# Performance work log

Hardware: AMD Instinct MI355X
Metric: run time of the kernel (lower is better)

Reference implementation:

```python
import jax, jax.numpy as jnp
import numpy as np

VOCAB, EMBED, EN_H, DE_H, ATTN, LAYERS = 50000, 256, 512, 512, 256, 2
SEQ, BATCH = 1024, 64

def setup_inputs() -> dict:
    key = jax.random.key(0)
    ks = jax.random.split(key, 20)
    n = lambda k, shp: jax.random.normal(k, shp, dtype=jnp.float32)
    inp = {
        "cur_input": jax.random.randint(ks[0], (BATCH,), 0, VOCAB, dtype=jnp.int64) if jax.config.jax_enable_x64 else jax.random.randint(ks[0], (BATCH,), 0, VOCAB, dtype=jnp.int32),
        "h0": n(ks[1], (LAYERS, BATCH, DE_H)),
        "c0": n(ks[2], (LAYERS, BATCH, DE_H)),
        "enc_states": n(ks[3], (SEQ, BATCH, EN_H)),
        "attention_mask": jnp.ones((BATCH, SEQ), dtype=jnp.float32),
        # parameters
        "emb_table": n(ks[4], (VOCAB, EMBED)) * 0.02,
        "attn_W": n(ks[5], (EN_H + DE_H, ATTN)) * 0.02,   # attention_model: Linear(en+de, attn, bias=False)
        "attn_v": n(ks[6], (ATTN,)) * 0.02,               # Linear(attn, 1, bias=False)
        "cg_W": n(ks[7], (DE_H + EMBED + EN_H, EN_H)) * 0.02,  # context gate
        "cg_b": jnp.zeros((EN_H,), dtype=jnp.float32),
        "Wih0": n(ks[8], (4 * DE_H, EN_H + EMBED)) * 0.02,
        "Whh0": n(ks[9], (4 * DE_H, DE_H)) * 0.02,
        "bih0": jnp.zeros((4 * DE_H,), dtype=jnp.float32),
        "bhh0": jnp.zeros((4 * DE_H,), dtype=jnp.float32),
        "Wih1": n(ks[10], (4 * DE_H, DE_H)) * 0.02,
        "Whh1": n(ks[11], (4 * DE_H, DE_H)) * 0.02,
        "bih1": jnp.zeros((4 * DE_H,), dtype=jnp.float32),
        "bhh1": jnp.zeros((4 * DE_H,), dtype=jnp.float32),
        "out_W": n(ks[12], (DE_H, VOCAB)) * 0.02,
        "out_b": jnp.zeros((VOCAB,), dtype=jnp.float32),
    }
    return inp

def _lstm_cell(x, h, c, Wih, Whh, bih, bhh):
    gates = x @ Wih.T + h @ Whh.T + bih + bhh  # (B, 4H), torch gate order i,f,g,o
    i, f, g, o = jnp.split(gates, 4, axis=-1)
    c_new = jax.nn.sigmoid(f) * c + jax.nn.sigmoid(i) * jnp.tanh(g)
    h_new = jax.nn.sigmoid(o) * jnp.tanh(c_new)
    return h_new, c_new

def reference(cur_input, h0, c0, enc_states, attention_mask,
              emb_table, attn_W, attn_v, cg_W, cg_b,
              Wih0, Whh0, bih0, bhh0, Wih1, Whh1, bih1, bhh1,
              out_W, out_b):
    S, B, _ = enc_states.shape
    dec = h0[-1]  # (B, DE_H)
    # Bahdanau attention: score over seq dim
    dec_b = jnp.broadcast_to(dec[None], (S, B, dec.shape[-1]))
    feat = jnp.tanh(jnp.concatenate([enc_states, dec_b], axis=-1) @ attn_W)  # (S,B,ATTN)
    e = feat @ attn_v  # (S,B)
    e = jnp.where(attention_mask.T > 0, e, jnp.float32(-1e9))
    alpha = jax.nn.softmax(e, axis=0)  # (S,B)
    ctx = jnp.einsum('sb,sbh->bh', alpha, enc_states)  # (B, EN_H)
    # embedding + context gate
    emb = emb_table[cur_input]  # (B, EMBED)
    gate = jax.nn.sigmoid(jnp.concatenate([dec, emb, ctx], axis=-1) @ cg_W + cg_b)
    ctx = gate * ctx
    x = jnp.concatenate([emb, ctx], axis=-1)  # (B, EMBED+EN_H)
    # two-layer single-step LSTM
    h1, c1 = _lstm_cell(x, h0[0], c0[0], Wih0, Whh0, bih0, bhh0)
    h2, c2 = _lstm_cell(h1, h0[1], c0[1], Wih1, Whh1, bih1, bhh1)
    out = h2 @ out_W + out_b  # (B, VOCAB)
    return out, jnp.stack([h1, h2]), jnp.stack([c1, c2])
```

## Files before the change

### kernel.cpp

```cpp
#include <hip/hip_runtime.h>
#include <math.h>


typedef __attribute__((ext_vector_type(8))) short short8;
typedef __attribute__((ext_vector_type(4))) float f32x4;

__device__ __forceinline__ float sigf(float x) { return 1.f / (1.f + expf(-x)); }

__device__ __forceinline__ unsigned short f2bf(float f) {
    unsigned int u = __builtin_bit_cast(unsigned int, f);
    unsigned int r = (u + 0x7fffu + ((u >> 16) & 1u)) >> 16;
    return (unsigned short)r;
}

__device__ __forceinline__ float tanh_fast(float x) {
    float t = __expf(2.f * x);
    return 1.f - 2.f * __builtin_amdgcn_rcpf(1.f + t);
}

__global__ void k_prep_conv(const int* __restrict__ cur, const float* __restrict__ h0,
                            const float* __restrict__ emb_table, const float* __restrict__ attn_W,
                            float* __restrict__ X1, float* __restrict__ X2, float* __restrict__ X3,
                            float* __restrict__ decW, unsigned short* __restrict__ Wt) {
    int t = threadIdx.x;
    if (blockIdx.x >= 64) {
        __shared__ float tile[64][65];
        int bx = blockIdx.x - 64;
        int kb = (bx & 7) * 64, nb = (bx >> 3) * 64;
        int r0 = t >> 6, c = t & 63;
#pragma unroll
        for (int i = 0; i < 16; ++i) {
            int r = i * 4 + r0;
            tile[r][c] = attn_W[(size_t)(kb + r) * 256 + nb + c];
        }
        __syncthreads();
#pragma unroll
        for (int i = 0; i < 16; ++i) {
            int r = i * 4 + r0;
            Wt[(size_t)(nb + r) * 512 + kb + c] = f2bf(tile[c][r]);
        }
        return;
    }
    __shared__ float dec_s[512];
    int b = blockIdx.x;
    const float* dec = h0 + (size_t)(64 + b) * 512;
    for (int i = t; i < 512; i += 256) {
        float v = dec[i];
        dec_s[i] = v;
        X1[b * 1280 + i] = v;
        X2[b * 1280 + 768 + i] = h0[(size_t)b * 512 + i];
        X3[b * 1024 + 512 + i] = v;
    }
    int row = cur[b];
    float ev = emb_table[(size_t)row * 256 + t];
    X1[b * 1280 + 512 + t] = ev;
    X2[b * 1280 + t] = ev;
    __syncthreads();
    float acc = 0.f;
    for (int k = 0; k < 512; ++k)
        acc += dec_s[k] * attn_W[(size_t)(512 + k) * 256 + t];
    decW[b * 256 + t] = acc;
}

__global__ __launch_bounds__(256) void k_scores_mfma(
        const float* __restrict__ enc, const unsigned short* __restrict__ Wt,
        const float* __restrict__ attn_v, const float* __restrict__ decW,
        float* __restrict__ e_out) {
    int s = blockIdx.x, t = threadIdx.x;
    __shared__ __align__(16) unsigned short sA[4096];
    __shared__ __align__(16) unsigned short sB[16384];
    const float* arow = enc + (size_t)s * 64 * 512;
    int w = t >> 6, l = t & 63, li = l & 15, lg = l >> 4;
    int sw = (li & 7) << 4;

    f32x4 acc[4][4];
#pragma unroll
    for (int rt = 0; rt < 4; ++rt)
#pragma unroll
        for (int ct = 0; ct < 4; ++ct) acc[rt][ct] = (f32x4){0.f, 0.f, 0.f, 0.f};

    for (int kk = 0; kk < 512; kk += 64) {
        __syncthreads();
#pragma unroll
        for (int i = 0; i < 2; ++i) {
            int idx = i * 256 + t, row = idx >> 3, kg = idx & 7;
            const float* g = arow + row * 512 + kk + kg * 8;
            float4 p0 = *(const float4*)g;
            float4 p1 = *(const float4*)(g + 4);
            uint4 wv;
            wv.x = f2bf(p0.x) | ((unsigned)f2bf(p0.y) << 16);
            wv.y = f2bf(p0.z) | ((unsigned)f2bf(p0.w) << 16);
            wv.z = f2bf(p1.x) | ((unsigned)f2bf(p1.y) << 16);
            wv.w = f2bf(p1.z) | ((unsigned)f2bf(p1.w) << 16);
            int byte = (row * 128 + kg * 16) ^ ((row & 7) << 4);
            *(uint4*)((char*)sA + byte) = wv;
        }
#pragma unroll
        for (int i = 0; i < 8; ++i) {
            int idx = i * 256 + t, n = idx >> 3, kg = idx & 7;
            uint4 wv = *(const uint4*)(Wt + (size_t)n * 512 + kk + kg * 8);
            int byte = (n * 128 + kg * 16) ^ ((n & 7) << 4);
            *(uint4*)((char*)sB + byte) = wv;
        }
        __syncthreads();
#pragma unroll
        for (int ks = 0; ks < 2; ++ks) {
            short8 af[4], bf[4];
#pragma unroll
            for (int rt = 0; rt < 4; ++rt) {
                int row = rt * 16 + li;
                af[rt] = *(short8*)((char*)sA + ((row * 128 + ks * 64 + lg * 16) ^ sw));
            }
#pragma unroll
            for (int ct = 0; ct < 4; ++ct) {
                int n = w * 64 + ct * 16 + li;
                bf[ct] = *(short8*)((char*)sB + ((n * 128 + ks * 64 + lg * 16) ^ sw));
            }
#pragma unroll
            for (int rt = 0; rt < 4; ++rt)
#pragma unroll
                for (int ct = 0; ct < 4; ++ct)
                    acc[rt][ct] = __builtin_amdgcn_mfma_f32_16x16x32_bf16(
                        af[rt], bf[ct], acc[rt][ct], 0, 0, 0);
        }
    }
    float er[4][4];
#pragma unroll
    for (int rt = 0; rt < 4; ++rt)
#pragma unroll
        for (int r = 0; r < 4; ++r) er[rt][r] = 0.f;
#pragma unroll
    for (int ct = 0; ct < 4; ++ct) {
        int a = w * 64 + ct * 16 + li;
        float v = attn_v[a];
#pragma unroll
        for (int rt = 0; rt < 4; ++rt) {
#pragma unroll
            for (int r = 0; r < 4; ++r) {
                int row = rt * 16 + lg * 4 + r;
                float x = acc[rt][ct][r] + decW[row * 256 + a];
                er[rt][r] += tanh_fast(x) * v;
            }
        }
    }
#pragma unroll
    for (int off = 1; off < 16; off <<= 1)
#pragma unroll
        for (int rt = 0; rt < 4; ++rt)
#pragma unroll
            for (int r = 0; r < 4; ++r)
                er[rt][r] += __shfl_xor(er[rt][r], off, 64);
    __syncthreads();
    float* part = (float*)sA;
    if (li == 0) {
#pragma unroll
        for (int rt = 0; rt < 4; ++rt)
#pragma unroll
            for (int r = 0; r < 4; ++r)
                part[w * 64 + rt * 16 + lg * 4 + r] = er[rt][r];
    }
    __syncthreads();
    if (t < 64)
        e_out[t * 1024 + s] = part[t] + part[64 + t] + part[128 + t] + part[192 + t];
}

__global__ __launch_bounds__(512) void k_ctx_partial(const float* __restrict__ ebuf,
        const float* __restrict__ mask, const float* __restrict__ enc,
        float* __restrict__ ctxP) {
    int b = blockIdx.x & 63, sc = blockIdx.x >> 6;
    int t = threadIdx.x;
    __shared__ float al[128];
    __shared__ float red[16];
    float v0 = ebuf[b * 1024 + t];
    float v1 = ebuf[b * 1024 + 512 + t];
    v0 = (mask[b * 1024 + t] > 0.f) ? v0 : -1e9f;
    v1 = (mask[b * 1024 + 512 + t] > 0.f) ? v1 : -1e9f;
    float lmax = fmaxf(v0, v1);
#pragma unroll
    for (int off = 32; off > 0; off >>= 1) lmax = fmaxf(lmax, __shfl_xor(lmax, off, 64));
    if ((t & 63) == 0) red[t >> 6] = lmax;
    __syncthreads();
    float m = red[0];
#pragma unroll
    for (int i = 1; i < 8; ++i) m = fmaxf(m, red[i]);
    float lsum = __expf(v0 - m) + __expf(v1 - m);
#pragma unroll
    for (int off = 32; off > 0; off >>= 1) lsum += __shfl_xor(lsum, off, 64);
    if ((t & 63) == 0) red[8 + (t >> 6)] = lsum;
    __syncthreads();
    float tot = red[8];
#pragma unroll
    for (int i = 1; i < 8; ++i) tot += red[8 + i];
    float inv = 1.f / tot;
    if (t < 128) {
        int s = sc * 128 + t;
        float x = ebuf[b * 1024 + s];
        x = (mask[b * 1024 + s] > 0.f) ? x : -1e9f;
        al[t] = __expf(x - m) * inv;
    }
    __syncthreads();
    const float* base = enc + (((size_t)sc * 128 * 64) + b) * 512 + t;
    float a0 = 0.f, a1 = 0.f, a2 = 0.f, a3 = 0.f;
    for (int s = 0; s < 128; s += 4) {
        float x0 = base[(size_t)(s + 0) * 32768];
        float x1 = base[(size_t)(s + 1) * 32768];
        float x2 = base[(size_t)(s + 2) * 32768];
        float x3 = base[(size_t)(s + 3) * 32768];
        a0 += al[s] * x0; a1 += al[s + 1] * x1; a2 += al[s + 2] * x2; a3 += al[s + 3] * x3;
    }
    ctxP[((size_t)sc * 64 + b) * 512 + t] = a0 + a1 + a2 + a3;
}

__global__ __launch_bounds__(1024) void k_gemm_cg(const float* __restrict__ X,
        const float* __restrict__ ctxP, const float* __restrict__ Wkn,
        float* __restrict__ P) {
    int n0 = blockIdx.x * 64, sp = blockIdx.y;
    int t = threadIdx.x, tc = t & 63, tr = t >> 6;
    __shared__ __align__(16) float As[64 * 68];
    __shared__ __align__(16) float Wc[64 * 68];
    float acc[4] = {0.f, 0.f, 0.f, 0.f};
    for (int c = 0; c < 5; ++c) {
        int k0 = sp * 320 + c * 64;
        __syncthreads();
#pragma unroll
        for (int i = 0; i < 4; ++i) {
            int idx = i * 1024 + t; int row = idx >> 6; int k = idx & 63;
            int gk = k0 + k;
            float v;
            if (gk < 768) {
                v = X[row * 1280 + gk];
            } else {
                int h = gk - 768;
                v = 0.f;
#pragma unroll
                for (int sc = 0; sc < 8; ++sc)
                    v += ctxP[((size_t)sc * 64 + row) * 512 + h];
            }
            As[k * 68 + row] = v;
        }
#pragma unroll
        for (int i = 0; i < 4; ++i) {
            int idx = i * 1024 + t; int k = idx >> 6; int cc = idx & 63;
            Wc[k * 68 + cc] = Wkn[(size_t)(k0 + k) * 512 + n0 + cc];
        }
        __syncthreads();
#pragma unroll 8
        for (int k = 0; k < 64; ++k) {
            float4 a = *(const float4*)&As[k * 68 + 4 * tr];
            float wv = Wc[k * 68 + tc];
            acc[0] += a.x * wv; acc[1] += a.y * wv; acc[2] += a.z * wv; acc[3] += a.w * wv;
        }
    }
    float* Pp = P + (size_t)sp * 64 * 512;
#pragma unroll
    for (int j = 0; j < 4; ++j) Pp[(4 * tr + j) * 512 + n0 + tc] = acc[j];
}

__global__ __launch_bounds__(1024) void k_gemm_lstm(const float* __restrict__ X, int ldx,
        const float* __restrict__ W1, int K1, const float* __restrict__ W2, int K2,
        int kchunks, float* __restrict__ P) {
    int n0 = blockIdx.x * 64, sp = blockIdx.y;
    int t = threadIdx.x, tc = t & 63, tr = t >> 6;
    __shared__ __align__(16) float As[64 * 68];
    __shared__ __align__(16) float Wc[64 * 68];
    float acc[4] = {0.f, 0.f, 0.f, 0.f};
    for (int c = 0; c < kchunks; ++c) {
        int k0 = (sp * kchunks + c) * 64;
        __syncthreads();
#pragma unroll
        for (int i = 0; i < 4; ++i) {
            int idx = i * 1024 + t; int row = idx >> 6; int k = idx & 63;
            As[k * 68 + row] = X[row * ldx + k0 + k];
        }
#pragma unroll
        for (int i = 0; i < 4; ++i) {
            int idx = i * 1024 + t; int cc = idx >> 6; int k = idx & 63;
            int gk = k0 + k; int j = n0 + cc;
            float wv = (gk < K1) ? W1[(size_t)j * K1 + gk] : W2[(size_t)j * K2 + gk - K1];
            Wc[k * 68 + cc] = wv;
        }
        __syncthreads();
#pragma unroll 8
        for (int k = 0; k < 64; ++k) {
            float4 a = *(const float4*)&As[k * 68 + 4 * tr];
            float wv = Wc[k * 68 + tc];
            acc[0] += a.x * wv; acc[1] += a.y * wv; acc[2] += a.z * wv; acc[3] += a.w * wv;
        }
    }
    float* Pp = P + (size_t)sp * 64 * 2048;
#pragma unroll
    for (int j = 0; j < 4; ++j) Pp[(4 * tr + j) * 2048 + n0 + tc] = acc[j];
}

__global__ void k_cg_fin(const float* __restrict__ P, const float* __restrict__ cg_b,
                         const float* __restrict__ ctxP, float* __restrict__ X2) {
    int idx = blockIdx.x * 256 + threadIdx.x;
    int b = idx >> 9, h = idx & 511;
    float g = cg_b[h];
#pragma unroll
    for (int sp = 0; sp < 4; ++sp) g += P[sp * 32768 + idx];
    float ctx = 0.f;
#pragma unroll
    for (int sc = 0; sc < 8; ++sc) ctx += ctxP[((size_t)sc * 64 + b) * 512 + h];
    X2[b * 1280 + 256 + h] = sigf(g) * ctx;
}

__global__ void k_lstm_fin(const float* __restrict__ P, const float* __restrict__ bih,
                           const float* __restrict__ bhh, const float* __restrict__ c0,
                           int layer, float* __restrict__ oh, float* __restrict__ oc,
                           float* __restrict__ X3out) {
    int idx = blockIdx.x * 256 + threadIdx.x;
    int b = idx >> 9, h = idx & 511;
    float gi = bih[h] + bhh[h];
    float gf = bih[512 + h] + bhh[512 + h];
    float gg = bih[1024 + h] + bhh[1024 + h];
    float go = bih[1536 + h] + bhh[1536 + h];
#pragma unroll
    for (int sp = 0; sp < 4; ++sp) {
        const float* Pp = P + sp * 131072 + b * 2048;
        gi += Pp[h]; gf += Pp[512 + h]; gg += Pp[1024 + h]; go += Pp[1536 + h];
    }
    float cp = c0[layer * 32768 + b * 512 + h];
    float cn = sigf(gf) * cp + sigf(gi) * tanhf(gg);
    float hn = sigf(go) * tanhf(cn);
    oh[b * 512 + h] = hn;
    oc[b * 512 + h] = cn;
    if (X3out) X3out[b * 1024 + h] = hn;
}

__global__ __launch_bounds__(256) void k_outproj_mfma(
        const float* __restrict__ h2, const float* __restrict__ out_W,
        const float* __restrict__ out_b, float* __restrict__ out) {
    int t = threadIdx.x;
    int n0 = blockIdx.x * 128;
    int w = t >> 6, l = t & 63, li = l & 15, lg = l >> 4;
    int sw = (li & 7) << 4;
    __shared__ __align__(16) unsigned short sA[4096];

    f32x4 acc[4][2];
#pragma unroll
    for (int rt = 0; rt < 4; ++rt)
#pragma unroll
        for (int ct = 0; ct < 2; ++ct) acc[rt][ct] = (f32x4){0.f, 0.f, 0.f, 0.f};
    int colbase = n0 + w * 32;

    for (int kk = 0; kk < 512; kk += 64) {
        __syncthreads();
#pragma unroll
        for (int i = 0; i < 2; ++i) {
            int idx = i * 256 + t, row = idx >> 3, kg = idx & 7;
            const float* g = h2 + row * 512 + kk + kg * 8;
            float4 p0 = *(const float4*)g;
            float4 p1 = *(const float4*)(g + 4);
            uint4 wv;
            wv.x = f2bf(p0.x) | ((unsigned)f2bf(p0.y) << 16);
            wv.y = f2bf(p0.z) | ((unsigned)f2bf(p0.w) << 16);
            wv.z = f2bf(p1.x) | ((unsigned)f2bf(p1.y) << 16);
            wv.w = f2bf(p1.z) | ((unsigned)f2bf(p1.w) << 16);
            int byte = (row * 128 + kg * 16) ^ ((row & 7) << 4);
            *(uint4*)((char*)sA + byte) = wv;
        }
        __syncthreads();
#pragma unroll
        for (int ks = 0; ks < 2; ++ks) {
            short8 bf[2];
#pragma unroll
            for (int ct = 0; ct < 2; ++ct) {
                int col = colbase + ct * 16 + li;
                col = (col < 50000) ? col : 49999;
                const float* wp = out_W + (size_t)(kk + ks * 32 + lg * 8) * 50000 + col;
                uint4 qv;
                float v0 = wp[0],          v1 = wp[50000];
                float v2 = wp[2 * 50000],  v3 = wp[3 * 50000];
                float v4 = wp[4 * 50000],  v5 = wp[5 * 50000];
                float v6 = wp[6 * 50000],  v7 = wp[7 * 50000];
                qv.x = f2bf(v0) | ((unsigned)f2bf(v1) << 16);
                qv.y = f2bf(v2) | ((unsigned)f2bf(v3) << 16);
                qv.z = f2bf(v4) | ((unsigned)f2bf(v5) << 16);
                qv.w = f2bf(v6) | ((unsigned)f2bf(v7) << 16);
                bf[ct] = *(short8*)&qv;
            }
            short8 af[4];
#pragma unroll
            for (int rt = 0; rt < 4; ++rt) {
                int row = rt * 16 + li;
                af[rt] = *(short8*)((char*)sA + ((row * 128 + ks * 64 + lg * 16) ^ sw));
            }
#pragma unroll
            for (int rt = 0; rt < 4; ++rt)
#pragma unroll
                for (int ct = 0; ct < 2; ++ct)
                    acc[rt][ct] = __builtin_amdgcn_mfma_f32_16x16x32_bf16(
                        af[rt], bf[ct], acc[rt][ct], 0, 0, 0);
        }
    }
#pragma unroll
    for (int ct = 0; ct < 2; ++ct) {
        int col = colbase + ct * 16 + li;
        if (col < 50000) {
            float bias = out_b[col];
#pragma unroll
            for (int rt = 0; rt < 4; ++rt)
#pragma unroll
                for (int r = 0; r < 4; ++r) {
                    int row = rt * 16 + lg * 4 + r;
                    out[(size_t)row * 50000 + col] = acc[rt][ct][r] + bias;
                }
        }
    }
}

extern "C" void kernel_launch(void* const* d_in, const int* in_sizes, int n_in,
                              void* d_out, int out_size, void* d_ws, size_t ws_size,
                              hipStream_t stream) {
    const int*   cur       = (const int*)d_in[0];
    const float* h0        = (const float*)d_in[1];
    const float* c0        = (const float*)d_in[2];
    const float* enc       = (const float*)d_in[3];
    const float* mask      = (const float*)d_in[4];
    const float* emb_table = (const float*)d_in[5];
    const float* attn_W    = (const float*)d_in[6];
    const float* attn_v    = (const float*)d_in[7];
    const float* cg_W      = (const float*)d_in[8];
    const float* cg_b      = (const float*)d_in[9];
    const float* Wih0      = (const float*)d_in[10];
    const float* Whh0      = (const float*)d_in[11];
    const float* bih0      = (const float*)d_in[12];
    const float* bhh0      = (const float*)d_in[13];
    const float* Wih1      = (const float*)d_in[14];
    const float* Whh1      = (const float*)d_in[15];
    const float* bih1      = (const float*)d_in[16];
    const float* bhh1      = (const float*)d_in[17];
    const float* out_W     = (const float*)d_in[18];
    const float* out_b     = (const float*)d_in[19];
    float* out = (float*)d_out;

    float* w    = (float*)d_ws;
    float* X1   = w;
    float* X2   = X1 + 81920;
    float* X3   = X2 + 81920;
    float* decW = X3 + 65536;
    float* eb   = decW + 16384;
    float* P    = eb + 65536;
    unsigned short* Wt = (unsigned short*)P;
    float* ctxP = P + 65536;
    ctxP = P + 524288;

    float* outH = out + 3200000;
    float* outC = out + 3265536;

    hipLaunchKernelGGL(k_prep_conv, dim3(96), dim3(256), 0, stream,
                       cur, h0, emb_table, attn_W, X1, X2, X3, decW, Wt);
    hipLaunchKernelGGL(k_scores_mfma, dim3(1024), dim3(256), 0, stream,
                       enc, Wt, attn_v, decW, eb);
    hipLaunchKernelGGL(k_ctx_partial, dim3(512), dim3(512), 0, stream,
                       eb, mask, enc, ctxP);
    hipLaunchKernelGGL(k_gemm_cg, dim3(8, 4), dim3(1024), 0, stream,
                       X1, ctxP, cg_W, P);
    hipLaunchKernelGGL(k_cg_fin, dim3(128), dim3(256), 0, stream, P, cg_b, ctxP, X2);
    hipLaunchKernelGGL(k_gemm_lstm, dim3(32, 4), dim3(1024), 0, stream,
                       X2, 1280, Wih0, 768, Whh0, 512, 5, P);
    hipLaunchKernelGGL(k_lstm_fin, dim3(128), dim3(256), 0, stream,
                       P, bih0, bhh0, c0, 0, outH, outC, X3);
    hipLaunchKernelGGL(k_gemm_lstm, dim3(32, 4), dim3(1024), 0, stream,
                       X3, 1024, Wih1, 512, Whh1, 512, 4, P);
    hipLaunchKernelGGL(k_lstm_fin, dim3(128), dim3(256), 0, stream,
                       P, bih1, bhh1, c0, 1, outH + 32768, outC + 32768, (float*)nullptr);
    hipLaunchKernelGGL(k_outproj_mfma, dim3(391), dim3(256), 0, stream,
                       outH + 32768, out_W, out_b, out);
}
```

Baseline: 187.7 us.

## Pre-swizzle attention weight, double scores tile to two seq rows, vectorise ctx

The prep kernel now writes the transposed bf16 attention weight in the XOR-swizzled LDS layout, so the scores kernel can copy it into shared memory with plain contiguous uint4 loads. Each scores block now covers two sequence positions (128 rows), which halves the grid and reuses each loaded B tile across twice as many MFMAs. The cost is a larger accumulator array and more register pressure. The context kernel switches to float4 loads with four sequence groups per block, combined by a shared-memory reduction.

```diff
diff --git a/kernel.cpp b/kernel.cpp
--- a/kernel.cpp
+++ b/kernel.cpp
@@ -37,7 +37,9 @@
 #pragma unroll
         for (int i = 0; i < 16; ++i) {
             int r = i * 4 + r0;
-            Wt[(size_t)(nb + r) * 512 + kb + c] = f2bf(tile[c][r]);
+            int n = nb + r;
+            int byte = ((n * 128 + ((c >> 3) << 4)) ^ ((r & 7) << 4)) + ((c & 7) << 1);
+            *(unsigned short*)((char*)Wt + kb * 512 + byte) = f2bf(tile[c][r]);
         }
         return;
     }
@@ -66,25 +68,25 @@
         const float* __restrict__ enc, const unsigned short* __restrict__ Wt,
         const float* __restrict__ attn_v, const float* __restrict__ decW,
         float* __restrict__ e_out) {
-    int s = blockIdx.x, t = threadIdx.x;
-    __shared__ __align__(16) unsigned short sA[4096];
+    int bid = blockIdx.x, t = threadIdx.x;
+    __shared__ __align__(16) unsigned short sA[8192];
     __shared__ __align__(16) unsigned short sB[16384];
-    const float* arow = enc + (size_t)s * 64 * 512;
+    const float* base = enc + (size_t)bid * 128 * 512;
     int w = t >> 6, l = t & 63, li = l & 15, lg = l >> 4;
     int sw = (li & 7) << 4;
 
-    f32x4 acc[4][4];
-#pragma unroll
-    for (int rt = 0; rt < 4; ++rt)
+    f32x4 acc[8][4];
+#pragma unroll
+    for (int rt = 0; rt < 8; ++rt)
 #pragma unroll
         for (int ct = 0; ct < 4; ++ct) acc[rt][ct] = (f32x4){0.f, 0.f, 0.f, 0.f};
 
     for (int kk = 0; kk < 512; kk += 64) {
         __syncthreads();
 #pragma unroll
-        for (int i = 0; i < 2; ++i) {
+        for (int i = 0; i < 4; ++i) {
             int idx = i * 256 + t, row = idx >> 3, kg = idx & 7;
-            const float* g = arow + row * 512 + kk + kg * 8;
+            const float* g = base + row * 512 + kk + kg * 8;
             float4 p0 = *(const float4*)g;
             float4 p1 = *(const float4*)(g + 4);
             uint4 wv;
@@ -95,38 +97,33 @@
             int byte = (row * 128 + kg * 16) ^ ((row & 7) << 4);
             *(uint4*)((char*)sA + byte) = wv;
         }
-#pragma unroll
-        for (int i = 0; i < 8; ++i) {
-            int idx = i * 256 + t, n = idx >> 3, kg = idx & 7;
-            uint4 wv = *(const uint4*)(Wt + (size_t)n * 512 + kk + kg * 8);
-            int byte = (n * 128 + kg * 16) ^ ((n & 7) << 4);
-            *(uint4*)((char*)sB + byte) = wv;
-        }
+        const uint4* src = (const uint4*)((const char*)Wt + (kk << 9));
+#pragma unroll
+        for (int i = 0; i < 8; ++i)
+            ((uint4*)sB)[i * 256 + t] = src[i * 256 + t];
         __syncthreads();
 #pragma unroll
         for (int ks = 0; ks < 2; ++ks) {
-            short8 af[4], bf[4];
-#pragma unroll
-            for (int rt = 0; rt < 4; ++rt) {
+            short8 af[8];
+#pragma unroll
+            for (int rt = 0; rt < 8; ++rt) {
                 int row = rt * 16 + li;
                 af[rt] = *(short8*)((char*)sA + ((row * 128 + ks * 64 + lg * 16) ^ sw));
             }
 #pragma unroll
             for (int ct = 0; ct < 4; ++ct) {
                 int n = w * 64 + ct * 16 + li;
-                bf[ct] = *(short8*)((char*)sB + ((n * 128 + ks * 64 + lg * 16) ^ sw));
-            }
-#pragma unroll
-            for (int rt = 0; rt < 4; ++rt)
-#pragma unroll
-                for (int ct = 0; ct < 4; ++ct)
+                short8 bf = *(short8*)((char*)sB + ((n * 128 + ks * 64 + lg * 16) ^ sw));
+#pragma unroll
+                for (int rt = 0; rt < 8; ++rt)
                     acc[rt][ct] = __builtin_amdgcn_mfma_f32_16x16x32_bf16(
-                        af[rt], bf[ct], acc[rt][ct], 0, 0, 0);
-        }
-    }
-    float er[4][4];
-#pragma unroll
-    for (int rt = 0; rt < 4; ++rt)
+                        af[rt], bf, acc[rt][ct], 0, 0, 0);
+            }
+        }
+    }
+    float er[8][4];
+#pragma unroll
+    for (int rt = 0; rt < 8; ++rt)
 #pragma unroll
         for (int r = 0; r < 4; ++r) er[rt][r] = 0.f;
 #pragma unroll
@@ -134,11 +131,11 @@
         int a = w * 64 + ct * 16 + li;
         float v = attn_v[a];
 #pragma unroll
-        for (int rt = 0; rt < 4; ++rt) {
+        for (int rt = 0; rt < 8; ++rt) {
 #pragma unroll
             for (int r = 0; r < 4; ++r) {
                 int row = rt * 16 + lg * 4 + r;
-                float x = acc[rt][ct][r] + decW[row * 256 + a];
+                float x = acc[rt][ct][r] + decW[(row & 63) * 256 + a];
                 er[rt][r] += tanh_fast(x) * v;
             }
         }
@@ -146,7 +143,7 @@
 #pragma unroll
     for (int off = 1; off < 16; off <<= 1)
 #pragma unroll
-        for (int rt = 0; rt < 4; ++rt)
+        for (int rt = 0; rt < 8; ++rt)
 #pragma unroll
             for (int r = 0; r < 4; ++r)
                 er[rt][r] += __shfl_xor(er[rt][r], off, 64);
@@ -154,14 +151,16 @@
     float* part = (float*)sA;
     if (li == 0) {
 #pragma unroll
-        for (int rt = 0; rt < 4; ++rt)
+        for (int rt = 0; rt < 8; ++rt)
 #pragma unroll
             for (int r = 0; r < 4; ++r)
-                part[w * 64 + rt * 16 + lg * 4 + r] = er[rt][r];
-    }
-    __syncthreads();
-    if (t < 64)
-        e_out[t * 1024 + s] = part[t] + part[64 + t] + part[128 + t] + part[192 + t];
+                part[w * 128 + rt * 16 + lg * 4 + r] = er[rt][r];
+    }
+    __syncthreads();
+    if (t < 128) {
+        float s = part[t] + part[128 + t] + part[256 + t] + part[384 + t];
+        e_out[(t & 63) * 1024 + 2 * bid + (t >> 6)] = s;
+    }
 }
 
 __global__ __launch_bounds__(512) void k_ctx_partial(const float* __restrict__ ebuf,
@@ -171,6 +170,7 @@
     int t = threadIdx.x;
     __shared__ float al[128];
     __shared__ float red[16];
+    __shared__ float4 red4[512];
     float v0 = ebuf[b * 1024 + t];
     float v1 = ebuf[b * 1024 + 512 + t];
     v0 = (mask[b * 1024 + t] > 0.f) ? v0 : -1e9f;
@@ -199,16 +199,24 @@
         al[t] = __expf(x - m) * inv;
     }
     __syncthreads();
-    const float* base = enc + (((size_t)sc * 128 * 64) + b) * 512 + t;
-    float a0 = 0.f, a1 = 0.f, a2 = 0.f, a3 = 0.f;
-    for (int s = 0; s < 128; s += 4) {
-        float x0 = base[(size_t)(s + 0) * 32768];
-        float x1 = base[(size_t)(s + 1) * 32768];
-        float x2 = base[(size_t)(s + 2) * 32768];
-        float x3 = base[(size_t)(s + 3) * 32768];
-        a0 += al[s] * x0; a1 += al[s + 1] * x1; a2 += al[s + 2] * x2; a3 += al[s + 3] * x3;
-    }
-    ctxP[((size_t)sc * 64 + b) * 512 + t] = a0 + a1 + a2 + a3;
+    int hv = t & 127, sg = t >> 7;
+    const float4* enc4 = (const float4*)enc;
+    float4 a = {0.f, 0.f, 0.f, 0.f};
+#pragma unroll 4
+    for (int j = 0; j < 32; ++j) {
+        int s = sg * 32 + j;
+        float4 x = enc4[(((size_t)(sc * 128 + s)) * 64 + b) * 128 + hv];
+        float wgt = al[s];
+        a.x += wgt * x.x; a.y += wgt * x.y; a.z += wgt * x.z; a.w += wgt * x.w;
+    }
+    red4[t] = a;
+    __syncthreads();
+    if (t < 128) {
+        float4 r0 = red4[t], r1 = red4[128 + t], r2 = red4[256 + t], r3 = red4[384 + t];
+        float4 o = {r0.x + r1.x + r2.x + r3.x, r0.y + r1.y + r2.y + r3.y,
+                    r0.z + r1.z + r2.z + r3.z, r0.w + r1.w + r2.w + r3.w};
+        ((float4*)ctxP)[((size_t)(sc * 64 + b)) * 128 + t] = o;
+    }
 }
 
 __global__ __launch_bounds__(1024) void k_gemm_cg(const float* __restrict__ X,
@@ -443,15 +451,14 @@
     float* eb   = decW + 16384;
     float* P    = eb + 65536;
     unsigned short* Wt = (unsigned short*)P;
-    float* ctxP = P + 65536;
-    ctxP = P + 524288;
+    float* ctxP = P + 524288;
 
     float* outH = out + 3200000;
     float* outC = out + 3265536;
 
     hipLaunchKernelGGL(k_prep_conv, dim3(96), dim3(256), 0, stream,
                        cur, h0, emb_table, attn_W, X1, X2, X3, decW, Wt);
-    hipLaunchKernelGGL(k_scores_mfma, dim3(1024), dim3(256), 0, stream,
+    hipLaunchKernelGGL(k_scores_mfma, dim3(512), dim3(256), 0, stream,
                        enc, Wt, attn_v, decW, eb);
     hipLaunchKernelGGL(k_ctx_partial, dim3(512), dim3(512), 0, stream,
                        eb, mask, enc, ctxP);
```

Result: slower. 202.5 us (+7.9%).

## Fuse context-gate and LSTM stages into one cooperative kernel; pre-swizzle attention weights

Applied to the files above, without the earlier changes.

Replaces six small kernel launches (context-gate GEMM, gate finalize, two LSTM GEMMs and two LSTM finalizes) with one cooperative kernel of 64 blocks that uses grid-wide syncs between stages. This is meant to remove per-launch overhead and the idle gaps between dependent kernels. The LSTM GEMMs now use 2 K-splits instead of 4, so each block does more serial K work and fewer blocks run. Separately, the prep kernel writes the transposed attention weight already in the swizzled LDS layout, so the scores kernel copies it straight into LDS without recomputing addresses.

```diff
diff --git a/kernel.cpp b/kernel.cpp
--- a/kernel.cpp
+++ b/kernel.cpp
@@ -1,5 +1,8 @@
 #include <hip/hip_runtime.h>
+#include <hip/hip_cooperative_groups.h>
 #include <math.h>
+
+namespace cg_ns = cooperative_groups;
 
 
 typedef __attribute__((ext_vector_type(8))) short short8;
@@ -37,7 +40,9 @@
 #pragma unroll
         for (int i = 0; i < 16; ++i) {
             int r = i * 4 + r0;
-            Wt[(size_t)(nb + r) * 512 + kb + c] = f2bf(tile[c][r]);
+            int n = nb + r;
+            int byte = ((n * 128 + ((c >> 3) << 4)) ^ ((r & 7) << 4)) + ((c & 7) << 1);
+            *(unsigned short*)((char*)Wt + kb * 512 + byte) = f2bf(tile[c][r]);
         }
         return;
     }
@@ -95,13 +100,10 @@
             int byte = (row * 128 + kg * 16) ^ ((row & 7) << 4);
             *(uint4*)((char*)sA + byte) = wv;
         }
-#pragma unroll
-        for (int i = 0; i < 8; ++i) {
-            int idx = i * 256 + t, n = idx >> 3, kg = idx & 7;
-            uint4 wv = *(const uint4*)(Wt + (size_t)n * 512 + kk + kg * 8);
-            int byte = (n * 128 + kg * 16) ^ ((n & 7) << 4);
-            *(uint4*)((char*)sB + byte) = wv;
-        }
+        const uint4* src = (const uint4*)((const char*)Wt + (kk << 9));
+#pragma unroll
+        for (int i = 0; i < 8; ++i)
+            ((uint4*)sB)[i * 256 + t] = src[i * 256 + t];
         __syncthreads();
 #pragma unroll
         for (int ks = 0; ks < 2; ++ks) {
@@ -211,121 +213,187 @@
     ctxP[((size_t)sc * 64 + b) * 512 + t] = a0 + a1 + a2 + a3;
 }
 
-__global__ __launch_bounds__(1024) void k_gemm_cg(const float* __restrict__ X,
-        const float* __restrict__ ctxP, const float* __restrict__ Wkn,
-        float* __restrict__ P) {
-    int n0 = blockIdx.x * 64, sp = blockIdx.y;
-    int t = threadIdx.x, tc = t & 63, tr = t >> 6;
+__global__ __launch_bounds__(1024) void k_chain(
+        const float* __restrict__ X1, const float* __restrict__ ctxP,
+        const float* __restrict__ cg_W, const float* __restrict__ cg_b,
+        const float* __restrict__ Wih0, const float* __restrict__ Whh0,
+        const float* __restrict__ bih0, const float* __restrict__ bhh0,
+        const float* __restrict__ Wih1, const float* __restrict__ Whh1,
+        const float* __restrict__ bih1, const float* __restrict__ bhh1,
+        const float* __restrict__ c0, float* __restrict__ P,
+        float* __restrict__ X2, float* __restrict__ X3,
+        float* __restrict__ outH, float* __restrict__ outC) {
+    cg_ns::grid_group grid = cg_ns::this_grid();
     __shared__ __align__(16) float As[64 * 68];
     __shared__ __align__(16) float Wc[64 * 68];
-    float acc[4] = {0.f, 0.f, 0.f, 0.f};
-    for (int c = 0; c < 5; ++c) {
-        int k0 = sp * 320 + c * 64;
-        __syncthreads();
-#pragma unroll
-        for (int i = 0; i < 4; ++i) {
-            int idx = i * 1024 + t; int row = idx >> 6; int k = idx & 63;
-            int gk = k0 + k;
-            float v;
-            if (gk < 768) {
-                v = X[row * 1280 + gk];
-            } else {
-                int h = gk - 768;
-                v = 0.f;
-#pragma unroll
-                for (int sc = 0; sc < 8; ++sc)
-                    v += ctxP[((size_t)sc * 64 + row) * 512 + h];
-            }
-            As[k * 68 + row] = v;
-        }
-#pragma unroll
-        for (int i = 0; i < 4; ++i) {
-            int idx = i * 1024 + t; int k = idx >> 6; int cc = idx & 63;
-            Wc[k * 68 + cc] = Wkn[(size_t)(k0 + k) * 512 + n0 + cc];
-        }
-        __syncthreads();
+    int t = threadIdx.x, tc = t & 63, tr = t >> 6;
+    int blk = blockIdx.x;
+
+    if (blk < 32) {
+        int n0 = (blk & 7) * 64, sp = blk >> 3;
+        float acc[4] = {0.f, 0.f, 0.f, 0.f};
+        for (int c = 0; c < 5; ++c) {
+            int k0 = sp * 320 + c * 64;
+            __syncthreads();
+#pragma unroll
+            for (int i = 0; i < 4; ++i) {
+                int idx = i * 1024 + t; int row = idx >> 6; int k = idx & 63;
+                int gk = k0 + k;
+                float v;
+                if (gk < 768) {
+                    v = X1[row * 1280 + gk];
+                } else {
+                    int h = gk - 768;
+                    v = 0.f;
+#pragma unroll
+                    for (int sc = 0; sc < 8; ++sc)
+                        v += ctxP[((size_t)sc * 64 + row) * 512 + h];
+                }
+                As[k * 68 + row] = v;
+            }
+#pragma unroll
+            for (int i = 0; i < 4; ++i) {
+                int idx = i * 1024 + t; int k = idx >> 6; int cc = idx & 63;
+                Wc[k * 68 + cc] = cg_W[(size_t)(k0 + k) * 512 + n0 + cc];
+            }
+            __syncthreads();
 #pragma unroll 8
-        for (int k = 0; k < 64; ++k) {
-            float4 a = *(const float4*)&As[k * 68 + 4 * tr];
-            float wv = Wc[k * 68 + tc];
-            acc[0] += a.x * wv; acc[1] += a.y * wv; acc[2] += a.z * wv; acc[3] += a.w * wv;
-        }
-    }
-    float* Pp = P + (size_t)sp * 64 * 512;
-#pragma unroll
-    for (int j = 0; j < 4; ++j) Pp[(4 * tr + j) * 512 + n0 + tc] = acc[j];
-}
-
-__global__ __launch_bounds__(1024) void k_gemm_lstm(const float* __restrict__ X, int ldx,
-        const float* __restrict__ W1, int K1, const float* __restrict__ W2, int K2,
-        int kchunks, float* __restrict__ P) {
-    int n0 = blockIdx.x * 64, sp = blockIdx.y;
-    int t = threadIdx.x, tc = t & 63, tr = t >> 6;
-    __shared__ __align__(16) float As[64 * 68];
-    __shared__ __align__(16) float Wc[64 * 68];
-    float acc[4] = {0.f, 0.f, 0.f, 0.f};
-    for (int c = 0; c < kchunks; ++c) {
-        int k0 = (sp * kchunks + c) * 64;
-        __syncthreads();
-#pragma unroll
-        for (int i = 0; i < 4; ++i) {
-            int idx = i * 1024 + t; int row = idx >> 6; int k = idx & 63;
-            As[k * 68 + row] = X[row * ldx + k0 + k];
-        }
-#pragma unroll
-        for (int i = 0; i < 4; ++i) {
-            int idx = i * 1024 + t; int cc = idx >> 6; int k = idx & 63;
-            int gk = k0 + k; int j = n0 + cc;
-            float wv = (gk < K1) ? W1[(size_t)j * K1 + gk] : W2[(size_t)j * K2 + gk - K1];
-            Wc[k * 68 + cc] = wv;
-        }
-        __syncthreads();
+            for (int k = 0; k < 64; ++k) {
+                float4 a = *(const float4*)&As[k * 68 + 4 * tr];
+                float wv = Wc[k * 68 + tc];
+                acc[0] += a.x * wv; acc[1] += a.y * wv; acc[2] += a.z * wv; acc[3] += a.w * wv;
+            }
+        }
+        float* Pp = P + (size_t)sp * 32768;
+#pragma unroll
+        for (int j = 0; j < 4; ++j) Pp[(4 * tr + j) * 512 + n0 + tc] = acc[j];
+    }
+    grid.sync();
+
+    {
+        int idx = blk * 1024 + t;
+        if (idx < 32768) {
+            int b = idx >> 9, h = idx & 511;
+            float g = cg_b[h];
+#pragma unroll
+            for (int sp = 0; sp < 4; ++sp) g += P[sp * 32768 + idx];
+            float ctx = 0.f;
+#pragma unroll
+            for (int sc = 0; sc < 8; ++sc) ctx += ctxP[((size_t)sc * 64 + b) * 512 + h];
+            X2[b * 1280 + 256 + h] = sigf(g) * ctx;
+        }
+    }
+    grid.sync();
+
+    {
+        int n0 = (blk & 31) * 64, sp = blk >> 5;
+        float acc[4] = {0.f, 0.f, 0.f, 0.f};
+        for (int c = 0; c < 10; ++c) {
+            int k0 = sp * 640 + c * 64;
+            __syncthreads();
+#pragma unroll
+            for (int i = 0; i < 4; ++i) {
+                int idx = i * 1024 + t; int row = idx >> 6; int k = idx & 63;
+                As[k * 68 + row] = X2[row * 1280 + k0 + k];
+            }
+#pragma unroll
+            for (int i = 0; i < 4; ++i) {
+                int idx = i * 1024 + t; int cc = idx >> 6; int k = idx & 63;
+                int gk = k0 + k; int j = n0 + cc;
+                float wv = (gk < 768) ? Wih0[(size_t)j * 768 + gk]
+                                      : Whh0[(size_t)j * 512 + gk - 768];
+                Wc[k * 68 + cc] = wv;
+            }
+            __syncthreads();
 #pragma unroll 8
-        for (int k = 0; k < 64; ++k) {
-            float4 a = *(const float4*)&As[k * 68 + 4 * tr];
-            float wv = Wc[k * 68 + tc];
-            acc[0] += a.x * wv; acc[1] += a.y * wv; acc[2] += a.z * wv; acc[3] += a.w * wv;
-        }
-    }
-    float* Pp = P + (size_t)sp * 64 * 2048;
-#pragma unroll
-    for (int j = 0; j < 4; ++j) Pp[(4 * tr + j) * 2048 + n0 + tc] = acc[j];
-}
-
-__global__ void k_cg_fin(const float* __restrict__ P, const float* __restrict__ cg_b,
-                         const float* __restrict__ ctxP, float* __restrict__ X2) {
-    int idx = blockIdx.x * 256 + threadIdx.x;
-    int b = idx >> 9, h = idx & 511;
-    float g = cg_b[h];
-#pragma unroll
-    for (int sp = 0; sp < 4; ++sp) g += P[sp * 32768 + idx];
-    float ctx = 0.f;
-#pragma unroll
-    for (int sc = 0; sc < 8; ++sc) ctx += ctxP[((size_t)sc * 64 + b) * 512 + h];
-    X2[b * 1280 + 256 + h] = sigf(g) * ctx;
-}
-
-__global__ void k_lstm_fin(const float* __restrict__ P, const float* __restrict__ bih,
-                           const float* __restrict__ bhh, const float* __restrict__ c0,
-                           int layer, float* __restrict__ oh, float* __restrict__ oc,
-                           float* __restrict__ X3out) {
-    int idx = blockIdx.x * 256 + threadIdx.x;
-    int b = idx >> 9, h = idx & 511;
-    float gi = bih[h] + bhh[h];
-    float gf = bih[512 + h] + bhh[512 + h];
-    float gg = bih[1024 + h] + bhh[1024 + h];
-    float go = bih[1536 + h] + bhh[1536 + h];
-#pragma unroll
-    for (int sp = 0; sp < 4; ++sp) {
-        const float* Pp = P + sp * 131072 + b * 2048;
-        gi += Pp[h]; gf += Pp[512 + h]; gg += Pp[1024 + h]; go += Pp[1536 + h];
-    }
-    float cp = c0[layer * 32768 + b * 512 + h];
-    float cn = sigf(gf) * cp + sigf(gi) * tanhf(gg);
-    float hn = sigf(go) * tanhf(cn);
-    oh[b * 512 + h] = hn;
-    oc[b * 512 + h] = cn;
-    if (X3out) X3out[b * 1024 + h] = hn;
+            for (int k = 0; k < 64; ++k) {
+                float4 a = *(const float4*)&As[k * 68 + 4 * tr];
+                float wv = Wc[k * 68 + tc];
+                acc[0] += a.x * wv; acc[1] += a.y * wv; acc[2] += a.z * wv; acc[3] += a.w * wv;
+            }
+        }
+        float* Pp = P + (size_t)sp * 131072;
+#pragma unroll
+        for (int j = 0; j < 4; ++j) Pp[(4 * tr + j) * 2048 + n0 + tc] = acc[j];
+    }
+    grid.sync();
+
+    {
+        int idx = blk * 1024 + t;
+        if (idx < 32768) {
+            int b = idx >> 9, h = idx & 511;
+            float gi = bih0[h] + bhh0[h];
+            float gf = bih0[512 + h] + bhh0[512 + h];
+            float gg = bih0[1024 + h] + bhh0[1024 + h];
+            float go = bih0[1536 + h] + bhh0[1536 + h];
+#pragma unroll
+            for (int sp = 0; sp < 2; ++sp) {
+                const float* Pp = P + sp * 131072 + b * 2048;
+                gi += Pp[h]; gf += Pp[512 + h]; gg += Pp[1024 + h]; go += Pp[1536 + h];
+            }
+            float cp = c0[b * 512 + h];
+            float cn = sigf(gf) * cp + sigf(gi) * tanhf(gg);
+            float hn = sigf(go) * tanhf(cn);
+            outH[b * 512 + h] = hn;
+            outC[b * 512 + h] = cn;
+            X3[b * 1024 + h] = hn;
+        }
+    }
+    grid.sync();
+
+    {
+        int n0 = (blk & 31) * 64, sp = blk >> 5;
+        float acc[4] = {0.f, 0.f, 0.f, 0.f};
+        for (int c = 0; c < 8; ++c) {
+            int k0 = sp * 512 + c * 64;
+            __syncthreads();
+#pragma unroll
+            for (int i = 0; i < 4; ++i) {
+                int idx = i * 1024 + t; int row = idx >> 6; int k = idx & 63;
+                As[k * 68 + row] = X3[row * 1024 + k0 + k];
+            }
+#pragma unroll
+            for (int i = 0; i < 4; ++i) {
+                int idx = i * 1024 + t; int cc = idx >> 6; int k = idx & 63;
+                int gk = k0 + k; int j = n0 + cc;
+                float wv = (gk < 512) ? Wih1[(size_t)j * 512 + gk]
+                                      : Whh1[(size_t)j * 512 + gk - 512];
+                Wc[k * 68 + cc] = wv;
+            }
+            __syncthreads();
+#pragma unroll 8
+            for (int k = 0; k < 64; ++k) {
+                float4 a = *(const float4*)&As[k * 68 + 4 * tr];
+                float wv = Wc[k * 68 + tc];
+                acc[0] += a.x * wv; acc[1] += a.y * wv; acc[2] += a.z * wv; acc[3] += a.w * wv;
+            }
+        }
+        float* Pp = P + (size_t)sp * 131072;
+#pragma unroll
+        for (int j = 0; j < 4; ++j) Pp[(4 * tr + j) * 2048 + n0 + tc] = acc[j];
+    }
+    grid.sync();
+
+    {
+        int idx = blk * 1024 + t;
+        if (idx < 32768) {
+            int b = idx >> 9, h = idx & 511;
+            float gi = bih1[h] + bhh1[h];
+            float gf = bih1[512 + h] + bhh1[512 + h];
+            float gg = bih1[1024 + h] + bhh1[1024 + h];
+            float go = bih1[1536 + h] + bhh1[1536 + h];
+#pragma unroll
+            for (int sp = 0; sp < 2; ++sp) {
+                const float* Pp = P + sp * 131072 + b * 2048;
+                gi += Pp[h]; gf += Pp[512 + h]; gg += Pp[1024 + h]; go += Pp[1536 + h];
+            }
+            float cp = c0[32768 + b * 512 + h];
+            float cn = sigf(gf) * cp + sigf(gi) * tanhf(gg);
+            float hn = sigf(go) * tanhf(cn);
+            outH[32768 + b * 512 + h] = hn;
+            outC[32768 + b * 512 + h] = cn;
+        }
+    }
 }
 
 __global__ __launch_bounds__(256) void k_outproj_mfma(
@@ -443,8 +511,7 @@
     float* eb   = decW + 16384;
     float* P    = eb + 65536;
     unsigned short* Wt = (unsigned short*)P;
-    float* ctxP = P + 65536;
-    ctxP = P + 524288;
+    float* ctxP = P + 524288;
 
     float* outH = out + 3200000;
     float* outC = out + 3265536;
@@ -455,17 +522,17 @@
                        enc, Wt, attn_v, decW, eb);
     hipLaunchKernelGGL(k_ctx_partial, dim3(512), dim3(512), 0, stream,
                        eb, mask, enc, ctxP);
-    hipLaunchKernelGGL(k_gemm_cg, dim3(8, 4), dim3(1024), 0, stream,
-                       X1, ctxP, cg_W, P);
-    hipLaunchKernelGGL(k_cg_fin, dim3(128), dim3(256), 0, stream, P, cg_b, ctxP, X2);
-    hipLaunchKernelGGL(k_gemm_lstm, dim3(32, 4), dim3(1024), 0, stream,
-                       X2, 1280, Wih0, 768, Whh0, 512, 5, P);
-    hipLaunchKernelGGL(k_lstm_fin, dim3(128), dim3(256), 0, stream,
-                       P, bih0, bhh0, c0, 0, outH, outC, X3);
-    hipLaunchKernelGGL(k_gemm_lstm, dim3(32, 4), dim3(1024), 0, stream,
-                       X3, 1024, Wih1, 512, Whh1, 512, 4, P);
-    hipLaunchKernelGGL(k_lstm_fin, dim3(128), dim3(256), 0, stream,
-                       P, bih1, bhh1, c0, 1, outH + 32768, outC + 32768, (float*)nullptr);
+    {
+        void* args[] = {
+            (void*)&X1, (void*)&ctxP, (void*)&cg_W, (void*)&cg_b,
+            (void*)&Wih0, (void*)&Whh0, (void*)&bih0, (void*)&bhh0,
+            (void*)&Wih1, (void*)&Whh1, (void*)&bih1, (void*)&bhh1,
+            (void*)&c0, (void*)&P, (void*)&X2, (void*)&X3,
+            (void*)&outH, (void*)&outC
+        };
+        hipLaunchCooperativeKernel((const void*)k_chain, dim3(64), dim3(1024),
+                                   args, 0, stream);
+    }
     hipLaunchKernelGGL(k_outproj_mfma, dim3(391), dim3(256), 0, stream,
                        outH + 32768, out_W, out_b, out);
 }
```

After: 284.6 us. 1.52x slower.

## Software-pipeline attention score GEMM with register prefetch and pre-swizzled weights

Applied to the files above, without the earlier changes.

The attention-score MFMA kernel now loads the next K-slice of encoder states and transposed weights into registers while the current slice is being multiplied. It double-buffers the A tile in shared memory and drops one barrier per iteration. The prep kernel writes the bf16 weight transpose in a pre-swizzled, chunked layout, so each warp copies its own contiguous slice of B into a warp-private region of shared memory and needs no cross-warp sync for it. The cost is more live registers for the prefetch buffers, which may lower occupancy.

```diff
diff --git a/kernel.cpp b/kernel.cpp
--- a/kernel.cpp
+++ b/kernel.cpp
@@ -37,7 +37,9 @@
 #pragma unroll
         for (int i = 0; i < 16; ++i) {
             int r = i * 4 + r0;
-            Wt[(size_t)(nb + r) * 512 + kb + c] = f2bf(tile[c][r]);
+            int n = nb + r;
+            int byte = ((n * 128 + ((c >> 3) << 4)) ^ ((r & 7) << 4)) + ((c & 7) << 1);
+            *(unsigned short*)((char*)Wt + kb * 512 + byte) = f2bf(tile[c][r]);
         }
         return;
     }
@@ -67,49 +69,76 @@
         const float* __restrict__ attn_v, const float* __restrict__ decW,
         float* __restrict__ e_out) {
     int s = blockIdx.x, t = threadIdx.x;
-    __shared__ __align__(16) unsigned short sA[4096];
+    __shared__ __align__(16) unsigned short sA[2][4096];
     __shared__ __align__(16) unsigned short sB[16384];
     const float* arow = enc + (size_t)s * 64 * 512;
     int w = t >> 6, l = t & 63, li = l & 15, lg = l >> 4;
     int sw = (li & 7) << 4;
 
+    int ar0 = t >> 3, akg0 = t & 7;
+    int ar1 = (256 + t) >> 3, akg1 = t & 7;
+    int abyte0 = (ar0 * 128 + akg0 * 16) ^ ((ar0 & 7) << 4);
+    int abyte1 = (ar1 * 128 + akg1 * 16) ^ ((ar1 & 7) << 4);
+    int bbase = w * 8192 + l * 16;
+
     f32x4 acc[4][4];
 #pragma unroll
     for (int rt = 0; rt < 4; ++rt)
 #pragma unroll
         for (int ct = 0; ct < 4; ++ct) acc[rt][ct] = (f32x4){0.f, 0.f, 0.f, 0.f};
 
-    for (int kk = 0; kk < 512; kk += 64) {
-        __syncthreads();
-#pragma unroll
-        for (int i = 0; i < 2; ++i) {
-            int idx = i * 256 + t, row = idx >> 3, kg = idx & 7;
-            const float* g = arow + row * 512 + kk + kg * 8;
-            float4 p0 = *(const float4*)g;
-            float4 p1 = *(const float4*)(g + 4);
-            uint4 wv;
-            wv.x = f2bf(p0.x) | ((unsigned)f2bf(p0.y) << 16);
-            wv.y = f2bf(p0.z) | ((unsigned)f2bf(p0.w) << 16);
-            wv.z = f2bf(p1.x) | ((unsigned)f2bf(p1.y) << 16);
-            wv.w = f2bf(p1.z) | ((unsigned)f2bf(p1.w) << 16);
-            int byte = (row * 128 + kg * 16) ^ ((row & 7) << 4);
-            *(uint4*)((char*)sA + byte) = wv;
-        }
-#pragma unroll
-        for (int i = 0; i < 8; ++i) {
-            int idx = i * 256 + t, n = idx >> 3, kg = idx & 7;
-            uint4 wv = *(const uint4*)(Wt + (size_t)n * 512 + kk + kg * 8);
-            int byte = (n * 128 + kg * 16) ^ ((n & 7) << 4);
-            *(uint4*)((char*)sB + byte) = wv;
-        }
-        __syncthreads();
+    float4 aP[4];
+    uint4  bP[8];
+
+#pragma unroll
+    for (int i = 0; i < 2; ++i) {
+        const float* g = arow + (ar0 + i * 32) * 512 + akg0 * 8;
+        aP[2 * i] = *(const float4*)g;
+        aP[2 * i + 1] = *(const float4*)(g + 4);
+    }
+#pragma unroll
+    for (int j = 0; j < 8; ++j)
+        bP[j] = *(const uint4*)((const char*)Wt + bbase + j * 1024);
+    {
+        uint4 wv0, wv1;
+        wv0.x = f2bf(aP[0].x) | ((unsigned)f2bf(aP[0].y) << 16);
+        wv0.y = f2bf(aP[0].z) | ((unsigned)f2bf(aP[0].w) << 16);
+        wv0.z = f2bf(aP[1].x) | ((unsigned)f2bf(aP[1].y) << 16);
+        wv0.w = f2bf(aP[1].z) | ((unsigned)f2bf(aP[1].w) << 16);
+        wv1.x = f2bf(aP[2].x) | ((unsigned)f2bf(aP[2].y) << 16);
+        wv1.y = f2bf(aP[2].z) | ((unsigned)f2bf(aP[2].w) << 16);
+        wv1.z = f2bf(aP[3].x) | ((unsigned)f2bf(aP[3].y) << 16);
+        wv1.w = f2bf(aP[3].z) | ((unsigned)f2bf(aP[3].w) << 16);
+        *(uint4*)((char*)sA[0] + abyte0) = wv0;
+        *(uint4*)((char*)sA[0] + abyte1) = wv1;
+#pragma unroll
+        for (int j = 0; j < 8; ++j)
+            *(uint4*)((char*)sB + bbase + j * 1024) = bP[j];
+    }
+    __syncthreads();
+
+    for (int kk = 0; kk < 8; ++kk) {
+        int cur = kk & 1;
+        if (kk < 7) {
+            int ko = (kk + 1) * 64;
+#pragma unroll
+            for (int i = 0; i < 2; ++i) {
+                const float* g = arow + (ar0 + i * 32) * 512 + ko + akg0 * 8;
+                aP[2 * i] = *(const float4*)g;
+                aP[2 * i + 1] = *(const float4*)(g + 4);
+            }
+            const char* src = (const char*)Wt + ((kk + 1) << 15);
+#pragma unroll
+            for (int j = 0; j < 8; ++j)
+                bP[j] = *(const uint4*)(src + bbase + j * 1024);
+        }
 #pragma unroll
         for (int ks = 0; ks < 2; ++ks) {
             short8 af[4], bf[4];
 #pragma unroll
             for (int rt = 0; rt < 4; ++rt) {
                 int row = rt * 16 + li;
-                af[rt] = *(short8*)((char*)sA + ((row * 128 + ks * 64 + lg * 16) ^ sw));
+                af[rt] = *(short8*)((char*)sA[cur] + ((row * 128 + ks * 64 + lg * 16) ^ sw));
             }
 #pragma unroll
             for (int ct = 0; ct < 4; ++ct) {
@@ -123,7 +152,25 @@
                     acc[rt][ct] = __builtin_amdgcn_mfma_f32_16x16x32_bf16(
                         af[rt], bf[ct], acc[rt][ct], 0, 0, 0);
         }
-    }
+        if (kk < 7) {
+            uint4 wv0, wv1;
+            wv0.x = f2bf(aP[0].x) | ((unsigned)f2bf(aP[0].y) << 16);
+            wv0.y = f2bf(aP[0].z) | ((unsigned)f2bf(aP[0].w) << 16);
+            wv0.z = f2bf(aP[1].x) | ((unsigned)f2bf(aP[1].y) << 16);
+            wv0.w = f2bf(aP[1].z) | ((unsigned)f2bf(aP[1].w) << 16);
+            wv1.x = f2bf(aP[2].x) | ((unsigned)f2bf(aP[2].y) << 16);
+            wv1.y = f2bf(aP[2].z) | ((unsigned)f2bf(aP[2].w) << 16);
+            wv1.z = f2bf(aP[3].x) | ((unsigned)f2bf(aP[3].y) << 16);
+            wv1.w = f2bf(aP[3].z) | ((unsigned)f2bf(aP[3].w) << 16);
+            *(uint4*)((char*)sA[cur ^ 1] + abyte0) = wv0;
+            *(uint4*)((char*)sA[cur ^ 1] + abyte1) = wv1;
+#pragma unroll
+            for (int j = 0; j < 8; ++j)
+                *(uint4*)((char*)sB + bbase + j * 1024) = bP[j];
+        }
+        __syncthreads();
+    }
+
     float er[4][4];
 #pragma unroll
     for (int rt = 0; rt < 4; ++rt)
@@ -150,8 +197,7 @@
 #pragma unroll
             for (int r = 0; r < 4; ++r)
                 er[rt][r] += __shfl_xor(er[rt][r], off, 64);
-    __syncthreads();
-    float* part = (float*)sA;
+    float* part = (float*)sA[0];
     if (li == 0) {
 #pragma unroll
         for (int rt = 0; rt < 4; ++rt)
@@ -443,8 +489,7 @@
     float* eb   = decW + 16384;
     float* P    = eb + 65536;
     unsigned short* Wt = (unsigned short*)P;
-    float* ctxP = P + 65536;
-    ctxP = P + 524288;
+    float* ctxP = P + 524288;
 
     float* outH = out + 3200000;
     float* outC = out + 3265536;
```

Measured after the change: 184.0 us. 1.02x faster.
